# Performance work log

Hardware: AMD Instinct MI355X
Metric: run time of the kernel (lower is better)

Reference implementation:

```python
import jax, jax.numpy as jnp
import numpy as np

N_NODES = 100000
N_EDGES = 1000000
D = 64
N_LAYERS = 3
LN_EPS = 1e-5


def setup_inputs() -> dict:
    key = jax.random.key(0)
    ks = jax.random.split(key, 12)
    s = 1.0 / np.sqrt(D)
    return {
        "feats": jax.random.normal(ks[0], (N_NODES, D), jnp.float32),
        "src": jax.random.randint(ks[1], (N_EDGES,), 0, N_NODES, jnp.int32),
        "dst": jax.random.randint(ks[2], (N_EDGES,), 0, N_NODES, jnp.int32),
        # GraphConv weights/biases (stacked over layers; in==hid==out==D)
        "conv_W": jax.random.normal(ks[3], (N_LAYERS, D, D), jnp.float32) * s,
        "conv_b": jnp.zeros((N_LAYERS, D), jnp.float32),
        # residual Linear per layer
        "res_W": jax.random.normal(ks[4], (N_LAYERS, D, D), jnp.float32) * s,
        "res_b": jnp.zeros((N_LAYERS, D), jnp.float32),
        # LayerNorm affine per layer
        "ln_g": jnp.ones((N_LAYERS, D), jnp.float32),
        "ln_b": jnp.zeros((N_LAYERS, D), jnp.float32),
        # final linear_prediction
        "pred_W": jax.random.normal(ks[5], (D, D), jnp.float32) * s,
        "pred_b": jnp.zeros((D,), jnp.float32),
    }


def _layer_norm(h, g, b):
    mu = jnp.mean(h, axis=-1, keepdims=True)
    var = jnp.mean(jnp.square(h - mu), axis=-1, keepdims=True)
    return (h - mu) * jax.lax.rsqrt(var + LN_EPS) * g + b


def reference(feats, src, dst, conv_W, conv_b, res_W, res_b, ln_g, ln_b, pred_W, pred_b):
    n = feats.shape[0]
    ones = jnp.ones(src.shape[0], feats.dtype)
    # DGL GraphConv norm='both', degrees clamped to >= 1
    out_deg = jnp.clip(jax.ops.segment_sum(ones, src, num_segments=n), 1.0, None)
    in_deg = jnp.clip(jax.ops.segment_sum(ones, dst, num_segments=n), 1.0, None)
    out_norm = jax.lax.rsqrt(out_deg)[:, None]  # [N,1]
    in_norm = jax.lax.rsqrt(in_deg)[:, None]

    h = feats
    h_final = jnp.zeros_like(feats)
    for i in range(N_LAYERS):
        # GraphConv: scale src, sum-aggregate over edges, scale dst, linear
        msg = (h * out_norm)[src]                                   # [E, D]
        agg = jax.ops.segment_sum(msg, dst, num_segments=n) * in_norm
        conv = agg @ conv_W[i] + conv_b[i]
        # residual linear + LayerNorm + relu (dropout p=0) + JK accumulate
        h = conv + h @ res_W[i] + res_b[i]
        h = jax.nn.relu(_layer_norm(h, ln_g[i], ln_b[i]))
        h_final = h_final + h
    return h_final @ pred_W + pred_b
```

## Files before the change

kernel.cpp:

```cpp
#include <hip/hip_runtime.h>
#include <hip/hip_bf16.h>

#define DD 64
#define NBLK 256
#define MAXBUK 1024
#define BSHIFT 7
#define NCTR 64

typedef __attribute__((ext_vector_type(8))) short short8v;
typedef __attribute__((ext_vector_type(4))) float f32x4;

__device__ __forceinline__ unsigned pk_bf16(float a, float b) {
    __hip_bfloat162 h = __float22bfloat162_rn(make_float2(a, b));
    unsigned u; __builtin_memcpy(&u, &h, 4); return u;
}
__device__ __forceinline__ short f2bf_s(float f) {
    union { float f; unsigned u; } x; x.f = f;
    unsigned r = x.u + 0x7fff + ((x.u >> 16) & 1);
    return (short)(r >> 16);
}
__device__ __forceinline__ float bf_lo(unsigned u) { return __int_as_float(u << 16); }
__device__ __forceinline__ float bf_hi(unsigned u) { return __int_as_float(u & 0xffff0000u); }
__device__ __forceinline__ short8v u4_to_s8(uint4 u) {
    union { uint4 u; short8v s; } x; x.u = u; return x.s;
}


__device__ void scan_bs(const int* __restrict__ bsums, int nb,
                        int* __restrict__ sbs, int* __restrict__ part) {
    int tid = threadIdx.x;
    int k = (nb + 255) >> 8;
    int base = tid * k;
    int s = 0;
    for (int j = 0; j < k; ++j) {
        int i = base + j;
        int v = (i < nb) ? bsums[i] : 0;
        sbs[i] = v;
        s += v;
    }
    part[tid] = s;
    __syncthreads();
    for (int off = 1; off < 256; off <<= 1) {
        int t = (tid >= off) ? part[tid - off] : 0;
        __syncthreads();
        part[tid] += t;
        __syncthreads();
    }
    int run = part[tid] - s;
    for (int j = 0; j < k; ++j) {
        int i = base + j;
        int v = sbs[i];
        sbs[i] = run;
        run += v;
    }
    __syncthreads();
}

__global__ __launch_bounds__(256) void part_count(
        const int* __restrict__ src, const int* __restrict__ dst,
        int* __restrict__ cnt, int* __restrict__ wctr, int E, int nbuk, int ce,
        int chunk) {
    __shared__ int hd[MAXBUK], hs[MAXBUK];
    if (blockIdx.x == 0) {
        for (int i = threadIdx.x; i < 3 * NCTR; i += 256)
            wctr[i * 32] = (i & (NCTR - 1)) * chunk;
    }
    for (int i = threadIdx.x; i < MAXBUK; i += 256) { hd[i] = 0; hs[i] = 0; }
    __syncthreads();
    int e0 = blockIdx.x * ce;
    int e1 = min(e0 + ce, E);
    for (int e = e0 + (int)threadIdx.x; e < e1; e += 256) {
        atomicAdd(&hd[dst[e] >> BSHIFT], 1);
        atomicAdd(&hs[src[e] >> BSHIFT], 1);
    }
    __syncthreads();
    int L2 = nbuk * NBLK;
    for (int b = threadIdx.x; b < nbuk; b += 256) {
        cnt[b * NBLK + blockIdx.x]      = hd[b];
        cnt[L2 + b * NBLK + blockIdx.x] = hs[b];
    }
}

__global__ void scan1p(int* __restrict__ a, int* __restrict__ bsums, int L) {
    __shared__ int tmp[256];
    int gid = blockIdx.x * 256 + threadIdx.x;
    int v = (gid < L) ? a[gid] : 0;
    tmp[threadIdx.x] = v;
    __syncthreads();
    for (int off = 1; off < 256; off <<= 1) {
        int t = (threadIdx.x >= off) ? tmp[threadIdx.x - off] : 0;
        __syncthreads();
        tmp[threadIdx.x] += t;
        __syncthreads();
    }
    if (gid < L) a[gid] = tmp[threadIdx.x] - v;
    if (threadIdx.x == 255) bsums[blockIdx.x] = tmp[255];
}

__global__ __launch_bounds__(256) void part_scatter(
        const int* __restrict__ src, const int* __restrict__ dst,
        const int* __restrict__ cnt, const int* __restrict__ bsums,
        unsigned int* __restrict__ partD, unsigned char* __restrict__ partS,
        int E, int nbuk, int ce, int nb) {
    __shared__ int cd[MAXBUK], cs[MAXBUK];
    __shared__ int sbs[2048], part[256];
    scan_bs(bsums, nb, sbs, part);
    int L2 = nbuk * NBLK;
    for (int b = threadIdx.x; b < nbuk; b += 256) {
        int i0 = b * NBLK + blockIdx.x;
        int i1 = L2 + b * NBLK + blockIdx.x;
        cd[b] = cnt[i0] + sbs[i0 >> 8];
        cs[b] = cnt[i1] + sbs[i1 >> 8] - E;
    }
    __syncthreads();
    int e0 = blockIdx.x * ce;
    int e1 = min(e0 + ce, E);
    for (int e = e0 + (int)threadIdx.x; e < e1; e += 256) {
        int s = src[e], d = dst[e];
        int pd = atomicAdd(&cd[d >> BSHIFT], 1);
        partD[pd] = ((unsigned)(d & 127) << 17) | (unsigned)s;
        int ps = atomicAdd(&cs[s >> BSHIFT], 1);
        partS[ps] = (unsigned char)(s & 127);
    }
}

__global__ __launch_bounds__(256) void bucket_all(
        const unsigned int* __restrict__ partD, const unsigned char* __restrict__ partS,
        const int* __restrict__ cnt, const int* __restrict__ bsums,
        const float* __restrict__ feats,
        int* __restrict__ rowptr, int* __restrict__ esrc,
        float* __restrict__ inn, float* __restrict__ outn, float* __restrict__ rs,
        unsigned short* __restrict__ hsv,
        int E, int nbuk, int n, int nb) {
    __shared__ int hi[128], sc[128], cu[128], ho[128];
    __shared__ float son[128];
    __shared__ int sbs[2048], part[256];
    scan_bs(bsums, nb, sbs, part);
    int b = blockIdx.x, tid = threadIdx.x;
    int L2 = nbuk * NBLK;
    int i0 = b * NBLK, i1 = (b + 1) * NBLK;
    int e0 = cnt[i0] + sbs[i0 >> 8];
    int e1 = (b + 1 < nbuk) ? (cnt[i1] + sbs[i1 >> 8]) : E;
    int f0 = cnt[L2 + i0] + sbs[(L2 + i0) >> 8] - E;
    int f1 = (b + 1 < nbuk) ? (cnt[L2 + i1] + sbs[(L2 + i1) >> 8] - E) : E;
    if (tid < 128) { hi[tid] = 0; ho[tid] = 0; }
    __syncthreads();
    for (int e = e0 + tid; e < e1; e += 256) atomicAdd(&hi[partD[e] >> 17], 1);
    for (int e = f0 + tid; e < f1; e += 256) atomicAdd(&ho[(int)partS[e]], 1);
    __syncthreads();
    if (tid < 128) sc[tid] = hi[tid];
    __syncthreads();
    for (int off = 1; off < 128; off <<= 1) {
        int t = (tid < 128 && tid >= off) ? sc[tid - off] : 0;
        __syncthreads();
        if (tid < 128) sc[tid] += t;
        __syncthreads();
    }
    int nodeBase = b << BSHIFT;
    if (tid < 128) {
        int excl = e0 + sc[tid] - hi[tid];
        cu[tid] = excl;
        float oc = (float)max(ho[tid], 1);
        float on = rsqrtf(oc);
        son[tid] = on;
        int v = nodeBase + tid;
        if (v < n) {
            rowptr[v] = excl;
            inn[v] = rsqrtf((float)max(hi[tid], 1));
            outn[v] = on;
            rs[v]   = sqrtf(oc);
        }
    }
    if (b == 0 && tid == 0) rowptr[n] = E;
    __syncthreads();
    for (int e = e0 + tid; e < e1; e += 256) {
        unsigned u = partD[e];
        int p = atomicAdd(&cu[u >> 17], 1);
        esrc[p] = (int)(u & 0x1FFFFu);
    }
    for (int idx = tid; idx < 128 * 8; idx += 256) {
        int vl = idx >> 3, c = idx & 7;
        int v = nodeBase + vl;
        if (v < n) {
            float s = son[vl];
            const float4* fp = (const float4*)(feats + (size_t)v * DD) + c * 2;
            float4 g0 = fp[0], g1 = fp[1];
            uint4 o;
            o.x = pk_bf16(g0.x * s, g0.y * s); o.y = pk_bf16(g0.z * s, g0.w * s);
            o.z = pk_bf16(g1.x * s, g1.y * s); o.w = pk_bf16(g1.z * s, g1.w * s);
            *(uint4*)&hsv[(size_t)v * DD + c * 8] = o;
        }
    }
}

__global__ __launch_bounds__(256) void gcn_kernel(
    const int* __restrict__ rowptr, const int* __restrict__ esrc,
    const float* __restrict__ inn, const float* __restrict__ rs,
    const float* __restrict__ outn,
    const unsigned short* __restrict__ hs_in,
    const float* __restrict__ Wc, const float* __restrict__ bc,
    const float* __restrict__ Wr, const float* __restrict__ br,
    const float* __restrict__ Wp, const float* __restrict__ pb,
    const float* __restrict__ g, const float* __restrict__ bb,
    unsigned short* __restrict__ hs_out, float* __restrict__ h_final,
    float* __restrict__ pred_out, int* __restrict__ wctr, int chunk,
    int first, int last, int n)
{
    __shared__ __align__(16) short sWf[24 * 64 * 8];
    __shared__ __align__(16) short sXa[4][16 * 72];
    __shared__ float sEps[4 * 64];

    int lane = threadIdx.x & 63;
    int wave = threadIdx.x >> 6;
    int q   = lane & 15;
    int gg  = lane >> 4;
    int q8  = lane & 7;
    int o8  = lane >> 3;

    for (int idx = threadIdx.x; idx < 64; idx += blockDim.x) {
        sEps[idx]       = bc[idx] + br[idx];
        sEps[64 + idx]  = g[idx];
        sEps[128 + idx] = bb[idx];
        sEps[192 + idx] = pb[idx];
    }
    for (int f = wave * 6; f < wave * 6 + 6; ++f) {
        int mat = f >> 3, ft = (f >> 1) & 3, kc = f & 1;
        const float* Ws = (mat == 0) ? Wc : (mat == 1) ? Wr : Wp;
        int feat = ft * 16 + q;
        int k0 = kc * 32 + gg * 8;
        short8v fr;
        #pragma unroll
        for (int j = 0; j < 8; ++j) fr[j] = f2bf_s(Ws[(k0 + j) * DD + feat]);
        *(short8v*)&sWf[(f * 64 + lane) * 8] = fr;
    }
    __syncthreads();

    short* xrow_w = &sXa[wave][0];
    const short8v* wf = (const short8v*)sWf;
    int ngrp = (n + 15) >> 4;

    int c = blockIdx.x & (NCTR - 1);
    int* ctr = wctr + c * 32;
    int lim = min((c + 1) * chunk, ngrp);

    int grp = 0;
    if (lane == 0) grp = atomicAdd(ctr, 1);
    grp = __shfl(grp, 0);

    while (grp < lim) {
        int gnext = 0;
        if (lane == 0) gnext = atomicAdd(ctr, 1);

        int vbase = grp << 4;
        int vo = vbase + q;
        int vsel = min(vo, n - 1);

        const uint4* hrow = (const uint4*)(hs_in + (size_t)vsel * DD);
        uint4 bh0u = hrow[gg];
        uint4 bh1u = hrow[4 + gg];
        float rsv  = rs[vsel];
        float innv = inn[vsel];

        int rp = rowptr[min(vbase + min(lane, 16), n)];
        int stA = __shfl(rp, o8);     int dgA = __shfl(rp, o8 + 1) - stA;
        int stB = __shfl(rp, o8 + 8); int dgB = __shfl(rp, o8 + 9) - stB;

        #pragma unroll
        for (int hh = 0; hh < 2; ++hh) {
            int st = hh ? stB : stA;
            int dg = hh ? dgB : dgA;
            int mdg = dg;
            mdg = max(mdg, __shfl_xor(mdg, 8));
            mdg = max(mdg, __shfl_xor(mdg, 16));
            mdg = max(mdg, __shfl_xor(mdg, 32));

            float a[8];
            #pragma unroll
            for (int cc = 0; cc < 8; ++cc) a[cc] = 0.0f;

            int id0 = (0 < dg) ? esrc[st + 0] : 0;  float m0 = (0 < dg) ? 1.f : 0.f;
            int id1 = (1 < dg) ? esrc[st + 1] : 0;  float m1 = (1 < dg) ? 1.f : 0.f;
            int id2 = (2 < dg) ? esrc[st + 2] : 0;  float m2 = (2 < dg) ? 1.f : 0.f;
            int id3 = (3 < dg) ? esrc[st + 3] : 0;  float m3 = (3 < dg) ? 1.f : 0.f;

            for (int t = 0; t < mdg; t += 4) {
                uint4 r0 = *(const uint4*)(hs_in + (size_t)id0 * DD + q8 * 8);
                uint4 r1 = *(const uint4*)(hs_in + (size_t)id1 * DD + q8 * 8);
                uint4 r2 = *(const uint4*)(hs_in + (size_t)id2 * DD + q8 * 8);
                uint4 r3 = *(const uint4*)(hs_in + (size_t)id3 * DD + q8 * 8);
                float c0 = m0, c1 = m1, c2 = m2, c3 = m3;
                int t4 = t + 4;
                id0 = (t4 + 0 < dg) ? esrc[st + t4 + 0] : 0;  m0 = (t4 + 0 < dg) ? 1.f : 0.f;
                id1 = (t4 + 1 < dg) ? esrc[st + t4 + 1] : 0;  m1 = (t4 + 1 < dg) ? 1.f : 0.f;
                id2 = (t4 + 2 < dg) ? esrc[st + t4 + 2] : 0;  m2 = (t4 + 2 < dg) ? 1.f : 0.f;
                id3 = (t4 + 3 < dg) ? esrc[st + t4 + 3] : 0;  m3 = (t4 + 3 < dg) ? 1.f : 0.f;
                a[0] = fmaf(bf_lo(r0.x), c0, a[0]); a[1] = fmaf(bf_hi(r0.x), c0, a[1]);
                a[2] = fmaf(bf_lo(r0.y), c0, a[2]); a[3] = fmaf(bf_hi(r0.y), c0, a[3]);
                a[4] = fmaf(bf_lo(r0.z), c0, a[4]); a[5] = fmaf(bf_hi(r0.z), c0, a[5]);
                a[6] = fmaf(bf_lo(r0.w), c0, a[6]); a[7] = fmaf(bf_hi(r0.w), c0, a[7]);
                a[0] = fmaf(bf_lo(r1.x), c1, a[0]); a[1] = fmaf(bf_hi(r1.x), c1, a[1]);
                a[2] = fmaf(bf_lo(r1.y), c1, a[2]); a[3] = fmaf(bf_hi(r1.y), c1, a[3]);
                a[4] = fmaf(bf_lo(r1.z), c1, a[4]); a[5] = fmaf(bf_hi(r1.z), c1, a[5]);
                a[6] = fmaf(bf_lo(r1.w), c1, a[6]); a[7] = fmaf(bf_hi(r1.w), c1, a[7]);
                a[0] = fmaf(bf_lo(r2.x), c2, a[0]); a[1] = fmaf(bf_hi(r2.x), c2, a[1]);
                a[2] = fmaf(bf_lo(r2.y), c2, a[2]); a[3] = fmaf(bf_hi(r2.y), c2, a[3]);
                a[4] = fmaf(bf_lo(r2.z), c2, a[4]); a[5] = fmaf(bf_hi(r2.z), c2, a[5]);
                a[6] = fmaf(bf_lo(r2.w), c2, a[6]); a[7] = fmaf(bf_hi(r2.w), c2, a[7]);
                a[0] = fmaf(bf_lo(r3.x), c3, a[0]); a[1] = fmaf(bf_hi(r3.x), c3, a[1]);
                a[2] = fmaf(bf_lo(r3.y), c3, a[2]); a[3] = fmaf(bf_hi(r3.y), c3, a[3]);
                a[4] = fmaf(bf_lo(r3.z), c3, a[4]); a[5] = fmaf(bf_hi(r3.z), c3, a[5]);
                a[6] = fmaf(bf_lo(r3.w), c3, a[6]); a[7] = fmaf(bf_hi(r3.w), c3, a[7]);
            }

            uint4 w4;
            w4.x = pk_bf16(a[0], a[1]); w4.y = pk_bf16(a[2], a[3]);
            w4.z = pk_bf16(a[4], a[5]); w4.w = pk_bf16(a[6], a[7]);
            *(uint4*)&xrow_w[(hh * 8 + o8) * 72 + q8 * 8] = w4;
        }

        const short* xr = &xrow_w[q * 72];
        short8v ba0 = *(const short8v*)&xr[gg * 8];
        short8v ba1 = *(const short8v*)&xr[32 + gg * 8];
        short8v sh0 = u4_to_s8(bh0u);
        short8v sh1 = u4_to_s8(bh1u);

        f32x4 accC[4], accR[4];
        #pragma unroll
        for (int ft = 0; ft < 4; ++ft) {
            f32x4 cq = {0.f, 0.f, 0.f, 0.f};
            cq = __builtin_amdgcn_mfma_f32_16x16x32_bf16(wf[(ft * 2 + 0) * 64 + lane], ba0, cq, 0, 0, 0);
            cq = __builtin_amdgcn_mfma_f32_16x16x32_bf16(wf[(ft * 2 + 1) * 64 + lane], ba1, cq, 0, 0, 0);
            accC[ft] = cq;
            f32x4 r = {0.f, 0.f, 0.f, 0.f};
            r = __builtin_amdgcn_mfma_f32_16x16x32_bf16(wf[(8 + ft * 2 + 0) * 64 + lane], sh0, r, 0, 0, 0);
            r = __builtin_amdgcn_mfma_f32_16x16x32_bf16(wf[(8 + ft * 2 + 1) * 64 + lane], sh1, r, 0, 0, 0);
            accR[ft] = r;
        }

        f32x4 ac[4];
        #pragma unroll
        for (int ft = 0; ft < 4; ++ft) {
            float4 b4 = *(const float4*)&sEps[ft * 16 + gg * 4];
            ac[ft][0] = fmaf(innv, accC[ft][0], fmaf(rsv, accR[ft][0], b4.x));
            ac[ft][1] = fmaf(innv, accC[ft][1], fmaf(rsv, accR[ft][1], b4.y));
            ac[ft][2] = fmaf(innv, accC[ft][2], fmaf(rsv, accR[ft][2], b4.z));
            ac[ft][3] = fmaf(innv, accC[ft][3], fmaf(rsv, accR[ft][3], b4.w));
        }
        float s = 0.f;
        #pragma unroll
        for (int ft = 0; ft < 4; ++ft) s += ac[ft][0] + ac[ft][1] + ac[ft][2] + ac[ft][3];
        s += __shfl_xor(s, 16); s += __shfl_xor(s, 32);
        float mu = s * (1.0f / 64.0f);
        float vsum = 0.f;
        #pragma unroll
        for (int ft = 0; ft < 4; ++ft) {
            #pragma unroll
            for (int r = 0; r < 4; ++r) { float d = ac[ft][r] - mu; vsum += d * d; }
        }
        vsum += __shfl_xor(vsum, 16); vsum += __shfl_xor(vsum, 32);
        float rinv = rsqrtf(vsum * (1.0f / 64.0f) + 1e-5f);

        float4 yv[4];
        #pragma unroll
        for (int ft = 0; ft < 4; ++ft) {
            float4 g4 = *(const float4*)&sEps[64 + ft * 16 + gg * 4];
            float4 c4 = *(const float4*)&sEps[128 + ft * 16 + gg * 4];
            yv[ft].x = fmaxf((ac[ft][0] - mu) * rinv * g4.x + c4.x, 0.f);
            yv[ft].y = fmaxf((ac[ft][1] - mu) * rinv * g4.y + c4.y, 0.f);
            yv[ft].z = fmaxf((ac[ft][2] - mu) * rinv * g4.z + c4.z, 0.f);
            yv[ft].w = fmaxf((ac[ft][3] - mu) * rinv * g4.w + c4.w, 0.f);
        }

        if (!last) {
            if (vo < n) {
                float on = outn[vo];
                #pragma unroll
                for (int ft = 0; ft < 4; ++ft) {
                    size_t off = (size_t)vo * DD + ft * 16 + gg * 4;
                    uint2 p;
                    p.x = pk_bf16(yv[ft].x * on, yv[ft].y * on);
                    p.y = pk_bf16(yv[ft].z * on, yv[ft].w * on);
                    *(uint2*)&hs_out[off] = p;
                    if (first) {
                        *(float4*)&h_final[off] = yv[ft];
                    } else {
                        float4 hf = *(const float4*)&h_final[off];
                        hf.x += yv[ft].x; hf.y += yv[ft].y;
                        hf.z += yv[ft].z; hf.w += yv[ft].w;
                        *(float4*)&h_final[off] = hf;
                    }
                }
            }
        } else {
            #pragma unroll
            for (int ft = 0; ft < 4; ++ft) {
                float4 hf = make_float4(0.f, 0.f, 0.f, 0.f);
                if (vo < n) {
                    float4 old = *(const float4*)&h_final[(size_t)vo * DD + ft * 16 + gg * 4];
                    hf.x = old.x + yv[ft].x; hf.y = old.y + yv[ft].y;
                    hf.z = old.z + yv[ft].z; hf.w = old.w + yv[ft].w;
                }
                uint2 p;
                p.x = pk_bf16(hf.x, hf.y);
                p.y = pk_bf16(hf.z, hf.w);
                *(uint2*)&xrow_w[q * 72 + ft * 16 + gg * 4] = p;
            }
            short8v bp0 = *(const short8v*)&xr[gg * 8];
            short8v bp1 = *(const short8v*)&xr[32 + gg * 8];
            #pragma unroll
            for (int ft = 0; ft < 4; ++ft) {
                f32x4 p = {0.f, 0.f, 0.f, 0.f};
                p = __builtin_amdgcn_mfma_f32_16x16x32_bf16(wf[(16 + ft * 2 + 0) * 64 + lane], bp0, p, 0, 0, 0);
                p = __builtin_amdgcn_mfma_f32_16x16x32_bf16(wf[(16 + ft * 2 + 1) * 64 + lane], bp1, p, 0, 0, 0);
                if (vo < n) {
                    float4 b4 = *(const float4*)&sEps[192 + ft * 16 + gg * 4];
                    float4 o = make_float4(p[0] + b4.x, p[1] + b4.y, p[2] + b4.z, p[3] + b4.w);
                    *(float4*)&pred_out[(size_t)vo * DD + ft * 16 + gg * 4] = o;
                }
            }
        }

        grp = __shfl(gnext, 0);
    }
}

extern "C" void kernel_launch(void* const* d_in, const int* in_sizes, int n_in,
                              void* d_out, int out_size, void* d_ws, size_t ws_size,
                              hipStream_t stream) {
    const float* feats  = (const float*)d_in[0];
    const int*   src    = (const int*)d_in[1];
    const int*   dst    = (const int*)d_in[2];
    const float* conv_W = (const float*)d_in[3];
    const float* conv_b = (const float*)d_in[4];
    const float* res_W  = (const float*)d_in[5];
    const float* res_b  = (const float*)d_in[6];
    const float* ln_g   = (const float*)d_in[7];
    const float* ln_b   = (const float*)d_in[8];
    const float* pred_W = (const float*)d_in[9];
    const float* pred_b = (const float*)d_in[10];

    int N = in_sizes[0] / DD;
    int E = in_sizes[1];

    int nbuk = (N + (1 << BSHIFT) - 1) >> BSHIFT;
    int ce   = (E + NBLK - 1) / NBLK;
    int L    = nbuk * NBLK * 2;
    int nb   = (L + 255) / 256;
    int ngrp = (N + 15) >> 4;
    int chunk = (ngrp + NCTR - 1) / NCTR;

    int*   rowptr = (int*)d_ws;
    int*   cnt    = rowptr + (N + 1);
    int*   bsA    = cnt + MAXBUK * NBLK * 2;
    int*   wctr   = bsA + 2048;
    int*   esrc   = wctr + 3 * NCTR * 32;
    float* outn   = (float*)(esrc + E);
    float* inn    = outn + N;
    float* rs     = inn + N;
    float* base   = (float*)(((uintptr_t)(rs + N) + 15) & ~(uintptr_t)15);
    unsigned short* hsA = (unsigned short*)base;
    unsigned short* hsB = (unsigned short*)(base + (size_t)N * 32);
    float* hfin  = base + (size_t)N * 64;
    unsigned int*  partD = (unsigned int*)hfin;
    unsigned char* partS = (unsigned char*)(partD + E);

    part_count  <<<NBLK, 256, 0, stream>>>(src, dst, cnt, wctr, E, nbuk, ce, chunk);
    scan1p      <<<nb, 256, 0, stream>>>(cnt, bsA, L);
    part_scatter<<<NBLK, 256, 0, stream>>>(src, dst, cnt, bsA, partD, partS, E, nbuk, ce, nb);
    bucket_all  <<<nbuk, 256, 0, stream>>>(partD, partS, cnt, bsA, feats, rowptr, esrc,
                                           inn, outn, rs, hsA, E, nbuk, N, nb);

    const unsigned short* ins[3]  = {hsA, hsB, hsA};
    unsigned short*       outs[3] = {hsB, hsA, hsB};
    for (int l = 0; l < 3; ++l) {
        gcn_kernel<<<1024, 256, 0, stream>>>(
            rowptr, esrc, inn, rs, outn, ins[l],
            conv_W + (size_t)l * DD * DD, conv_b + (size_t)l * DD,
            res_W  + (size_t)l * DD * DD, res_b  + (size_t)l * DD,
            pred_W, pred_b,
            ln_g   + (size_t)l * DD,      ln_b   + (size_t)l * DD,
            outs[l], hfin, (float*)d_out, wctr + l * NCTR * 32, chunk,
            (l == 0) ? 1 : 0, (l == 2) ? 1 : 0, N);
    }
}
```

Measured before the change: 285.5 us.

## Replace atomic work-stealing counters with static one-group-per-wave grid mapping

Removes the per-layer atomic work counters that waves used to fetch 16-node groups dynamically. The grid is now sized so each wave gets a fixed group index via a grid-stride loop. This drops atomic traffic and the counter initialization in part_count. In exchange it loses dynamic load balancing and amortizes per-block weight staging over fewer groups.

```diff
diff --git a/kernel.cpp b/kernel.cpp
--- a/kernel.cpp
+++ b/kernel.cpp
@@ -5,7 +5,6 @@
 #define NBLK 256
 #define MAXBUK 1024
 #define BSHIFT 7
-#define NCTR 64
 
 typedef __attribute__((ext_vector_type(8))) short short8v;
 typedef __attribute__((ext_vector_type(4))) float f32x4;
@@ -58,13 +57,8 @@
 
 __global__ __launch_bounds__(256) void part_count(
         const int* __restrict__ src, const int* __restrict__ dst,
-        int* __restrict__ cnt, int* __restrict__ wctr, int E, int nbuk, int ce,
-        int chunk) {
+        int* __restrict__ cnt, int E, int nbuk, int ce) {
     __shared__ int hd[MAXBUK], hs[MAXBUK];
-    if (blockIdx.x == 0) {
-        for (int i = threadIdx.x; i < 3 * NCTR; i += 256)
-            wctr[i * 32] = (i & (NCTR - 1)) * chunk;
-    }
     for (int i = threadIdx.x; i < MAXBUK; i += 256) { hd[i] = 0; hs[i] = 0; }
     __syncthreads();
     int e0 = blockIdx.x * ce;
@@ -203,7 +197,7 @@
     const float* __restrict__ Wp, const float* __restrict__ pb,
     const float* __restrict__ g, const float* __restrict__ bb,
     unsigned short* __restrict__ hs_out, float* __restrict__ h_final,
-    float* __restrict__ pred_out, int* __restrict__ wctr, int chunk,
+    float* __restrict__ pred_out,
     int first, int last, int n)
 {
     __shared__ __align__(16) short sWf[24 * 64 * 8];
@@ -237,20 +231,11 @@
 
     short* xrow_w = &sXa[wave][0];
     const short8v* wf = (const short8v*)sWf;
+    int wgid = blockIdx.x * 4 + wave;
+    int nwav = gridDim.x * 4;
     int ngrp = (n + 15) >> 4;
 
-    int c = blockIdx.x & (NCTR - 1);
-    int* ctr = wctr + c * 32;
-    int lim = min((c + 1) * chunk, ngrp);
-
-    int grp = 0;
-    if (lane == 0) grp = atomicAdd(ctr, 1);
-    grp = __shfl(grp, 0);
-
-    while (grp < lim) {
-        int gnext = 0;
-        if (lane == 0) gnext = atomicAdd(ctr, 1);
-
+    for (int grp = wgid; grp < ngrp; grp += nwav) {
         int vbase = grp << 4;
         int vo = vbase + q;
         int vsel = min(vo, n - 1);
@@ -419,8 +404,6 @@
                 }
             }
         }
-
-        grp = __shfl(gnext, 0);
     }
 }
 
@@ -447,13 +430,12 @@
     int L    = nbuk * NBLK * 2;
     int nb   = (L + 255) / 256;
     int ngrp = (N + 15) >> 4;
-    int chunk = (ngrp + NCTR - 1) / NCTR;
+    int gblk = (ngrp + 3) / 4;
 
     int*   rowptr = (int*)d_ws;
     int*   cnt    = rowptr + (N + 1);
     int*   bsA    = cnt + MAXBUK * NBLK * 2;
-    int*   wctr   = bsA + 2048;
-    int*   esrc   = wctr + 3 * NCTR * 32;
+    int*   esrc   = bsA + 2048;
     float* outn   = (float*)(esrc + E);
     float* inn    = outn + N;
     float* rs     = inn + N;
@@ -464,7 +446,7 @@
     unsigned int*  partD = (unsigned int*)hfin;
     unsigned char* partS = (unsigned char*)(partD + E);
 
-    part_count  <<<NBLK, 256, 0, stream>>>(src, dst, cnt, wctr, E, nbuk, ce, chunk);
+    part_count  <<<NBLK, 256, 0, stream>>>(src, dst, cnt, E, nbuk, ce);
     scan1p      <<<nb, 256, 0, stream>>>(cnt, bsA, L);
     part_scatter<<<NBLK, 256, 0, stream>>>(src, dst, cnt, bsA, partD, partS, E, nbuk, ce, nb);
     bucket_all  <<<nbuk, 256, 0, stream>>>(partD, partS, cnt, bsA, feats, rowptr, esrc,
@@ -473,13 +455,13 @@
     const unsigned short* ins[3]  = {hsA, hsB, hsA};
     unsigned short*       outs[3] = {hsB, hsA, hsB};
     for (int l = 0; l < 3; ++l) {
-        gcn_kernel<<<1024, 256, 0, stream>>>(
+        gcn_kernel<<<gblk, 256, 0, stream>>>(
             rowptr, esrc, inn, rs, outn, ins[l],
             conv_W + (size_t)l * DD * DD, conv_b + (size_t)l * DD,
             res_W  + (size_t)l * DD * DD, res_b  + (size_t)l * DD,
             pred_W, pred_b,
             ln_g   + (size_t)l * DD,      ln_b   + (size_t)l * DD,
-            outs[l], hfin, (float*)d_out, wctr + l * NCTR * 32, chunk,
+            outs[l], hfin, (float*)d_out,
             (l == 0) ? 1 : 0, (l == 2) ? 1 : 0, N);
     }
 }
```

Result: slower. 304.8 us (+6.8%).
